# Performance work log

Hardware: AMD Instinct MI355X
Metric: run time of the kernel (lower is better)

The kernel has to match this reference:

```python
import jax, jax.numpy as jnp
import numpy as np

D_MODEL = 1024

def setup_inputs() -> dict:
    key = jax.random.key(0)
    ks = jax.random.split(key, 7)
    scale = 1.0 / np.sqrt(D_MODEL)
    x = jax.random.normal(ks[0], (4, 2048, D_MODEL), dtype=jnp.float32)
    # nn.Linear weights are [out, in]; init uniform(-1/sqrt(in), 1/sqrt(in))
    wq = jax.random.uniform(ks[1], (D_MODEL, D_MODEL), jnp.float32, -scale, scale)
    wk = jax.random.uniform(ks[2], (D_MODEL, D_MODEL), jnp.float32, -scale, scale)
    wv = jax.random.uniform(ks[3], (D_MODEL, D_MODEL), jnp.float32, -scale, scale)
    bq = jax.random.uniform(ks[4], (D_MODEL,), jnp.float32, -scale, scale)
    bk = jax.random.uniform(ks[5], (D_MODEL,), jnp.float32, -scale, scale)
    bv = jax.random.uniform(ks[6], (D_MODEL,), jnp.float32, -scale, scale)
    return {"x": x, "wq": wq, "bq": bq, "wk": wk, "bk": bk, "wv": wv, "bv": bv}

def reference(x, wq, bq, wk, bk, wv, bv):
    B, T, C = x.shape
    q = jnp.einsum('btc,dc->btd', x, wq) + bq  # Linear: x @ W^T + b
    k = jnp.einsum('btc,dc->btd', x, wk) + bk
    v = jnp.einsum('btc,dc->btd', x, wv) + bv
    scores = jnp.einsum('bqd,bkd->bqk', q, k) / jnp.sqrt(jnp.float32(C))
    causal = jnp.tril(jnp.ones((T, T), dtype=bool))  # True = keep
    scores = jnp.where(causal, scores, jnp.finfo(scores.dtype).min)
    attn = jax.nn.softmax(scores, axis=-1)
    return jnp.einsum('bqk,bkd->bqd', attn, v)
```

## Files before the change

### kernel.cpp

```cpp
#include <hip/hip_runtime.h>
#include <math.h>

#define BATCH 4
#define SEQ   2048
#define DM    1024
#define NTOK  (BATCH * SEQ)

typedef __attribute__((ext_vector_type(8))) short bf16x8;
typedef __attribute__((ext_vector_type(4))) float f32x4;
typedef unsigned short u16;
struct alignas(8) us4 { u16 x, y, z, w; };

__device__ __forceinline__ u16 f2bf(float f) {
    union { float f; unsigned u; } v; v.f = f;
    unsigned r = v.u + 0x7fffu + ((v.u >> 16) & 1u);
    return (u16)(r >> 16);
}

__device__ __forceinline__ void gload_lds16(const void* g, void* l) {
    __builtin_amdgcn_global_load_lds(
        (const __attribute__((address_space(1))) unsigned int*)g,
        (__attribute__((address_space(3))) unsigned int*)l, 16, 0, 0);
}

__device__ __forceinline__ void stage_tile(
    const u16* __restrict__ G, int ld, int row0, int kt,
    u16* lds, int wid, int lane)
{
    #pragma unroll
    for (int j = 0; j < 2; ++j) {
        const int off  = wid * 2048 + j * 1024;
        const int loff = off + lane * 16;
        const int row  = loff >> 6;
        const int ke   = (loff & 63) >> 1;
        gload_lds16(G + (size_t)(row0 + row) * ld + kt + ke, (char*)lds + off);
    }
}

__device__ __forceinline__ void frag_mma(
    const u16* As, const u16* Bs, int wr, int wc, int lane, f32x4 acc[4][4])
{
    const int lrow = lane & 15, lk = (lane >> 4) * 8;
    bf16x8 a[4], b[4];
    #pragma unroll
    for (int i = 0; i < 4; ++i)
        a[i] = *(const bf16x8*)(As + (wr * 64 + i * 16 + lrow) * 32 + lk);
    #pragma unroll
    for (int i = 0; i < 4; ++i)
        b[i] = *(const bf16x8*)(Bs + (wc * 64 + i * 16 + lrow) * 32 + lk);
    #pragma unroll
    for (int i = 0; i < 4; ++i)
        #pragma unroll
        for (int j = 0; j < 4; ++j)
            acc[i][j] = __builtin_amdgcn_mfma_f32_16x16x32_bf16(
                a[i], b[j], acc[i][j], 0, 0, 0);
}

__global__ __launch_bounds__(256) void conv_all(
    const float* __restrict__ x,
    const float* __restrict__ w0, const float* __restrict__ w1,
    const float* __restrict__ w2,
    u16* __restrict__ xo,
    u16* __restrict__ o0, u16* __restrict__ o1, u16* __restrict__ o2)
{
    const int z = blockIdx.z;
    const float* in = (z == 0) ? x : (z == 1) ? w0 : (z == 2) ? w1 : w2;
    u16* out = (z == 0) ? xo : (z == 1) ? o0 : (z == 2) ? o1 : o2;
    const int n4 = (z == 0) ? (NTOK * DM / 4) : (DM * DM / 4);
    for (int i = blockIdx.x * 256 + threadIdx.x; i < n4; i += gridDim.x * 256) {
        float4 f = ((const float4*)in)[i];
        us4 p{f2bf(f.x), f2bf(f.y), f2bf(f.z), f2bf(f.w)};
        ((us4*)out)[i] = p;
    }
}

__global__ __launch_bounds__(256, 3) void qkv_mfma(
    const u16* __restrict__ xb,
    const u16* __restrict__ wqb, const float* __restrict__ bq,
    const u16* __restrict__ wkb, const float* __restrict__ bk,
    const u16* __restrict__ wvb, const float* __restrict__ bv,
    u16* __restrict__ qb, u16* __restrict__ kb, u16* __restrict__ vT)
{
    __shared__ u16 As[128 * 32], Bs[128 * 32];
    const int z = blockIdx.z;
    const u16* W = (z == 0) ? wqb : (z == 1) ? wkb : wvb;
    const float* bias = (z == 0) ? bq : (z == 1) ? bk : bv;
    const int m0 = blockIdx.x * 128, n0 = blockIdx.y * 128;
    const int t = threadIdx.x, wid = t >> 6, lane = t & 63;
    const int wr = wid >> 1, wc = wid & 1;

    f32x4 acc[4][4] = {};
    for (int kt = 0; kt < DM; kt += 32) {
        __syncthreads();
        stage_tile(xb, DM, m0, kt, As, wid, lane);
        stage_tile(W,  DM, n0, kt, Bs, wid, lane);
        __syncthreads();
        frag_mma(As, Bs, wr, wc, lane, acc);
    }

    const int lrow = lane & 15, lg = lane >> 4;
    if (z < 2) {
        u16* out = (z == 0) ? qb : kb;
        #pragma unroll
        for (int ni = 0; ni < 4; ++ni) {
            const int n = n0 + wc * 64 + ni * 16 + lrow;
            const float bn = bias[n];
            #pragma unroll
            for (int mi = 0; mi < 4; ++mi) {
                const int mb = m0 + wr * 64 + mi * 16 + lg * 4;
                #pragma unroll
                for (int r = 0; r < 4; ++r)
                    out[(size_t)(mb + r) * DM + n] = f2bf(acc[mi][ni][r] + bn);
            }
        }
    } else {
        #pragma unroll
        for (int ni = 0; ni < 4; ++ni) {
            const int n = n0 + wc * 64 + ni * 16 + lrow;
            const float bn = bias[n];
            #pragma unroll
            for (int mi = 0; mi < 4; ++mi) {
                const int mb = m0 + wr * 64 + mi * 16 + lg * 4;
                us4 p{f2bf(acc[mi][ni][0] + bn), f2bf(acc[mi][ni][1] + bn),
                      f2bf(acc[mi][ni][2] + bn), f2bf(acc[mi][ni][3] + bn)};
                *(us4*)(vT + (size_t)n * NTOK + mb) = p;
            }
        }
    }
}

__global__ __launch_bounds__(256, 3) void qk_exp(
    const u16* __restrict__ qb, const u16* __restrict__ kb,
    u16* __restrict__ attn, float* __restrict__ psum)
{
    const int m0 = blockIdx.x * 128, n0 = blockIdx.y * 128;
    if (n0 > m0) return;
    __shared__ u16 As[128 * 32], Bs[128 * 32];
    const int b = blockIdx.z;
    const u16* A = qb + (size_t)b * SEQ * DM;
    const u16* B = kb + (size_t)b * SEQ * DM;
    u16* P = attn + (size_t)b * SEQ * SEQ;
    const int t = threadIdx.x, wid = t >> 6, lane = t & 63;
    const int wr = wid >> 1, wc = wid & 1;

    f32x4 acc[4][4] = {};
    for (int kt = 0; kt < DM; kt += 32) {
        __syncthreads();
        stage_tile(A, DM, m0, kt, As, wid, lane);
        stage_tile(B, DM, n0, kt, Bs, wid, lane);
        __syncthreads();
        frag_mma(As, Bs, wr, wc, lane, acc);
    }
    const int lrow = lane & 15, lg = lane >> 4;
    const float scale = 0.03125f;
    const int nb = (n0 >> 6) | wc;
    #pragma unroll
    for (int mi = 0; mi < 4; ++mi) {
        #pragma unroll
        for (int r = 0; r < 4; ++r) {
            const int row = m0 + wr * 64 + mi * 16 + lg * 4 + r;
            float ps = 0.f;
            #pragma unroll
            for (int ni = 0; ni < 4; ++ni) {
                const int n = n0 + wc * 64 + ni * 16 + lrow;
                const float p = (n <= row) ? __expf(acc[mi][ni][r] * scale) : 0.f;
                P[(size_t)row * SEQ + n] = f2bf(p);
                ps += p;
            }
            #pragma unroll
            for (int mk = 1; mk < 16; mk <<= 1) ps += __shfl_xor(ps, mk);
            if (lrow == 0)
                psum[((size_t)b * SEQ + row) * 32 + nb] = ps;
        }
    }
}

__global__ __launch_bounds__(256, 3) void pv_mfma(
    const u16* __restrict__ attn, const u16* __restrict__ vT,
    const float* __restrict__ psum, float* __restrict__ out)
{
    __shared__ u16 As[128 * 32], Bs[128 * 32];
    __shared__ float invs[128];
    const int m0 = blockIdx.x * 128, n0 = blockIdx.y * 128;
    const int b = blockIdx.z;
    const u16* A = attn + (size_t)b * SEQ * SEQ;
    const u16* B = vT + (size_t)b * SEQ;
    float* C = out + (size_t)b * SEQ * DM;
    const int t = threadIdx.x, wid = t >> 6, lane = t & 63;
    const int wr = wid >> 1, wc = wid & 1;

    if (t < 128) {
        const int row = m0 + t;
        const float* pr = psum + ((size_t)b * SEQ + row) * 32;
        const int nbmax = (row >> 6) | 1;
        float s = 0.f;
        for (int nbi = 0; nbi <= nbmax; ++nbi) s += pr[nbi];
        invs[t] = 1.f / s;
    }

    f32x4 acc[4][4] = {};
    const int kmax = m0 + 128;
    for (int kt = 0; kt < kmax; kt += 32) {
        __syncthreads();
        stage_tile(A, SEQ,  m0, kt, As, wid, lane);
        stage_tile(B, NTOK, n0, kt, Bs, wid, lane);
        __syncthreads();
        frag_mma(As, Bs, wr, wc, lane, acc);
    }
    const int lrow = lane & 15, lg = lane >> 4;
    #pragma unroll
    for (int mi = 0; mi < 4; ++mi) {
        const int ml = wr * 64 + mi * 16 + lg * 4;
        #pragma unroll
        for (int ni = 0; ni < 4; ++ni) {
            const int n = n0 + wc * 64 + ni * 16 + lrow;
            #pragma unroll
            for (int r = 0; r < 4; ++r)
                C[(size_t)(m0 + ml + r) * DM + n] = acc[mi][ni][r] * invs[ml + r];
        }
    }
}

extern "C" void kernel_launch(void* const* d_in, const int* in_sizes, int n_in,
                              void* d_out, int out_size, void* d_ws, size_t ws_size,
                              hipStream_t stream)
{
    const float* x  = (const float*)d_in[0];
    const float* wq = (const float*)d_in[1];
    const float* bq = (const float*)d_in[2];
    const float* wk = (const float*)d_in[3];
    const float* bk = (const float*)d_in[4];
    const float* wv = (const float*)d_in[5];
    const float* bv = (const float*)d_in[6];
    float* out = (float*)d_out;

    u16* ws  = (u16*)d_ws;
    u16* xb  = ws;
    u16* wqb = xb  + (size_t)NTOK * DM;
    u16* wkb = wqb + (size_t)DM * DM;
    u16* wvb = wkb + (size_t)DM * DM;
    u16* qb  = wvb + (size_t)DM * DM;
    u16* kb  = qb  + (size_t)NTOK * DM;
    u16* vT  = kb  + (size_t)NTOK * DM;
    u16* attn = vT + (size_t)NTOK * DM;
    float* psum = (float*)(attn + (size_t)BATCH * SEQ * SEQ);

    conv_all<<<dim3(512, 1, 4), 256, 0, stream>>>(
        x, wq, wk, wv, xb, wqb, wkb, wvb);

    qkv_mfma<<<dim3(NTOK / 128, DM / 128, 3), 256, 0, stream>>>(
        xb, wqb, bq, wkb, bk, wvb, bv, qb, kb, vT);

    qk_exp<<<dim3(SEQ / 128, SEQ / 128, BATCH), 256, 0, stream>>>(
        qb, kb, attn, psum);

    pv_mfma<<<dim3(SEQ / 128, DM / 128, BATCH), 256, 0, stream>>>(
        attn, vT, psum, out);
}
```

Before: 177.9 us.

## Rewrite QKV projection GEMM as 256x128 double-buffered 8-wave pipelined kernel

Replaces the 128x128, single-buffered QKV projection kernel with a 512-thread kernel computing 256x128 tiles using a K-step of 64. It double-buffers shared memory, uses XOR-swizzled LDS layouts and overlaps async global-to-LDS loads with MFMA phases through explicit vmcnt waits, barriers and setprio. The aim is to hide load latency, cut LDS bank conflicts and raise reuse per tile in the largest GEMM. The cost is more LDS per block, lower occupancy, and hand-tuned waitcnt logic that must stay correct.

Result: slower. 188.9 us (+6.2%).

```diff
diff --git a/kernel.cpp b/kernel.cpp
--- a/kernel.cpp
+++ b/kernel.cpp
@@ -22,6 +22,163 @@
         (const __attribute__((address_space(1))) unsigned int*)g,
         (__attribute__((address_space(3))) unsigned int*)l, 16, 0, 0);
 }
+
+
+__device__ __forceinline__ void stageA(const u16* __restrict__ G, int ld,
+    int row0, int kt, u16* Ab, int h, int wid, int lane)
+{
+    #pragma unroll
+    for (int rr = 0; rr < 2; ++rr) {
+        const int base = h * 16384 + rr * 8192 + wid * 1024;
+        const int off  = base + lane * 16;
+        const int row  = off >> 7;
+        const int cbs  = (off & 127) ^ ((row & 7) << 4);
+        gload_lds16(G + (size_t)(row0 + row) * ld + kt + (cbs >> 1),
+                    (char*)Ab + base);
+    }
+}
+__device__ __forceinline__ void stageB(const u16* __restrict__ G, int ld,
+    int row0, int kt, u16* Bb, int h, int wid, int lane)
+{
+    const int base = h * 8192 + wid * 1024;
+    const int off  = base + lane * 16;
+    const int row  = off >> 7;
+    const int cbs  = (off & 127) ^ ((row & 7) << 4);
+    gload_lds16(G + (size_t)(row0 + row) * ld + kt + (cbs >> 1),
+                (char*)Bb + base);
+}
+
+struct Frags { bf16x8 a[2][4]; bf16x8 b[2]; };
+
+template<int MH, int NH>
+__device__ __forceinline__ Frags phase_read(const u16* As, const u16* Bs,
+                                            int wr, int wc, int lane)
+{
+    Frags fr;
+    const int lrow = lane & 15, lhi = lane >> 4, sw = (lane & 7) << 4;
+    #pragma unroll
+    for (int kk = 0; kk < 2; ++kk) {
+        const int cb = (kk * 64 + lhi * 16) ^ sw;
+        #pragma unroll
+        for (int fi = 0; fi < 4; ++fi) {
+            const int row = (2 * (MH * 4 + fi) + wr) * 16 + lrow;
+            fr.a[kk][fi] = *(const bf16x8*)(As + row * 64 + (cb >> 1));
+        }
+        const int nrow = (4 * NH + wc) * 16 + lrow;
+        fr.b[kk] = *(const bf16x8*)(Bs + nrow * 64 + (cb >> 1));
+    }
+    return fr;
+}
+
+template<int MH, int NH>
+__device__ __forceinline__ void phase_fma(const Frags& fr, f32x4 acc[8][2])
+{
+    __builtin_amdgcn_s_setprio(1);
+    #pragma unroll
+    for (int fi = 0; fi < 4; ++fi)
+        #pragma unroll
+        for (int kk = 0; kk < 2; ++kk)
+            acc[MH * 4 + fi][NH] = __builtin_amdgcn_mfma_f32_16x16x32_bf16(
+                fr.a[kk][fi], fr.b[kk], acc[MH * 4 + fi][NH], 0, 0, 0);
+    __builtin_amdgcn_s_setprio(0);
+}
+
+#define VM3 asm volatile("s_waitcnt vmcnt(3)" ::: "memory")
+#define VM0 asm volatile("s_waitcnt vmcnt(0)" ::: "memory")
+#define BAR __builtin_amdgcn_s_barrier()
+
+__global__ __launch_bounds__(512) void qkv_mfma8(
+    const u16* __restrict__ xb,
+    const u16* __restrict__ wqb, const float* __restrict__ bq,
+    const u16* __restrict__ wkb, const float* __restrict__ bk,
+    const u16* __restrict__ wvb, const float* __restrict__ bv,
+    u16* __restrict__ qb, u16* __restrict__ kb, u16* __restrict__ vT)
+{
+    __shared__ u16 As0[256 * 64], As1[256 * 64];
+    __shared__ u16 Bs0[128 * 64], Bs1[128 * 64];
+
+    const int z = blockIdx.z;
+    const u16* W = (z == 0) ? wqb : (z == 1) ? wkb : wvb;
+    const float* bias = (z == 0) ? bq : (z == 1) ? bk : bv;
+    const int m0 = blockIdx.x * 256;
+    const int n0 = blockIdx.y * 128;
+    const int t = threadIdx.x, wid = t >> 6, lane = t & 63;
+    const int wr = wid >> 2, wc = wid & 3;
+
+    f32x4 acc[8][2] = {};
+
+    stageA(xb, DM, m0, 0,  As0, 0, wid, lane);
+    stageB(W,  DM, n0, 0,  Bs0, 0, wid, lane);
+    stageA(xb, DM, m0, 0,  As0, 1, wid, lane);
+    stageB(W,  DM, n0, 0,  Bs0, 1, wid, lane);
+    stageA(xb, DM, m0, 64, As1, 0, wid, lane);
+    stageB(W,  DM, n0, 64, Bs1, 0, wid, lane);
+    VM3;
+    BAR;
+
+    #pragma unroll 1
+    for (int i = 0; i < 8; ++i) {
+        const int kb2 = i * 128 + 64, k2 = i * 128 + 128, k3 = i * 128 + 192;
+        const bool s2 = (k2 < 1024), s3 = (k3 < 1024);
+        { Frags fr = phase_read<0,0>(As0, Bs0, wr, wc, lane);
+          stageA(xb, DM, m0, kb2, As1, 1, wid, lane);
+          BAR; phase_fma<0,0>(fr, acc); BAR; }
+        { Frags fr = phase_read<0,1>(As0, Bs0, wr, wc, lane);
+          stageB(W, DM, n0, kb2, Bs1, 1, wid, lane);
+          BAR; phase_fma<0,1>(fr, acc); BAR; }
+        { Frags fr = phase_read<1,0>(As0, Bs0, wr, wc, lane);
+          if (s2) stageA(xb, DM, m0, k2, As0, 0, wid, lane);
+          BAR; phase_fma<1,0>(fr, acc); BAR; }
+        { Frags fr = phase_read<1,1>(As0, Bs0, wr, wc, lane);
+          if (s2) { stageB(W, DM, n0, k2, Bs0, 0, wid, lane); VM3; }
+          else    { VM0; }
+          BAR; phase_fma<1,1>(fr, acc); BAR; }
+        { Frags fr = phase_read<0,0>(As1, Bs1, wr, wc, lane);
+          if (s2) stageA(xb, DM, m0, k2, As0, 1, wid, lane);
+          BAR; phase_fma<0,0>(fr, acc); BAR; }
+        { Frags fr = phase_read<0,1>(As1, Bs1, wr, wc, lane);
+          if (s2) stageB(W, DM, n0, k2, Bs0, 1, wid, lane);
+          BAR; phase_fma<0,1>(fr, acc); BAR; }
+        { Frags fr = phase_read<1,0>(As1, Bs1, wr, wc, lane);
+          if (s3) stageA(xb, DM, m0, k3, As1, 0, wid, lane);
+          BAR; phase_fma<1,0>(fr, acc); BAR; }
+        { Frags fr = phase_read<1,1>(As1, Bs1, wr, wc, lane);
+          if (s3) { stageB(W, DM, n0, k3, Bs1, 0, wid, lane); VM3; }
+          else    { VM0; }
+          BAR; phase_fma<1,1>(fr, acc); BAR; }
+    }
+
+    const int lrow = lane & 15, lhi = lane >> 4;
+    if (z < 2) {
+        u16* outp = (z == 0) ? qb : kb;
+        #pragma unroll
+        for (int g = 0; g < 2; ++g) {
+            const int n = n0 + (4 * g + wc) * 16 + lrow;
+            const float bn = bias[n];
+            #pragma unroll
+            for (int f = 0; f < 8; ++f) {
+                const int mb = m0 + (2 * f + wr) * 16 + lhi * 4;
+                #pragma unroll
+                for (int r = 0; r < 4; ++r)
+                    outp[(size_t)(mb + r) * DM + n] = f2bf(acc[f][g][r] + bn);
+            }
+        }
+    } else {
+        #pragma unroll
+        for (int g = 0; g < 2; ++g) {
+            const int n = n0 + (4 * g + wc) * 16 + lrow;
+            const float bn = bias[n];
+            #pragma unroll
+            for (int f = 0; f < 8; ++f) {
+                const int mb = m0 + (2 * f + wr) * 16 + lhi * 4;
+                us4 p{f2bf(acc[f][g][0] + bn), f2bf(acc[f][g][1] + bn),
+                      f2bf(acc[f][g][2] + bn), f2bf(acc[f][g][3] + bn)};
+                *(us4*)(vT + (size_t)n * NTOK + mb) = p;
+            }
+        }
+    }
+}
+
 
 __device__ __forceinline__ void stage_tile(
     const u16* __restrict__ G, int ld, int row0, int kt,
@@ -71,61 +228,6 @@
         float4 f = ((const float4*)in)[i];
         us4 p{f2bf(f.x), f2bf(f.y), f2bf(f.z), f2bf(f.w)};
         ((us4*)out)[i] = p;
-    }
-}
-
-__global__ __launch_bounds__(256, 3) void qkv_mfma(
-    const u16* __restrict__ xb,
-    const u16* __restrict__ wqb, const float* __restrict__ bq,
-    const u16* __restrict__ wkb, const float* __restrict__ bk,
-    const u16* __restrict__ wvb, const float* __restrict__ bv,
-    u16* __restrict__ qb, u16* __restrict__ kb, u16* __restrict__ vT)
-{
-    __shared__ u16 As[128 * 32], Bs[128 * 32];
-    const int z = blockIdx.z;
-    const u16* W = (z == 0) ? wqb : (z == 1) ? wkb : wvb;
-    const float* bias = (z == 0) ? bq : (z == 1) ? bk : bv;
-    const int m0 = blockIdx.x * 128, n0 = blockIdx.y * 128;
-    const int t = threadIdx.x, wid = t >> 6, lane = t & 63;
-    const int wr = wid >> 1, wc = wid & 1;
-
-    f32x4 acc[4][4] = {};
-    for (int kt = 0; kt < DM; kt += 32) {
-        __syncthreads();
-        stage_tile(xb, DM, m0, kt, As, wid, lane);
-        stage_tile(W,  DM, n0, kt, Bs, wid, lane);
-        __syncthreads();
-        frag_mma(As, Bs, wr, wc, lane, acc);
-    }
-
-    const int lrow = lane & 15, lg = lane >> 4;
-    if (z < 2) {
-        u16* out = (z == 0) ? qb : kb;
-        #pragma unroll
-        for (int ni = 0; ni < 4; ++ni) {
-            const int n = n0 + wc * 64 + ni * 16 + lrow;
-            const float bn = bias[n];
-            #pragma unroll
-            for (int mi = 0; mi < 4; ++mi) {
-                const int mb = m0 + wr * 64 + mi * 16 + lg * 4;
-                #pragma unroll
-                for (int r = 0; r < 4; ++r)
-                    out[(size_t)(mb + r) * DM + n] = f2bf(acc[mi][ni][r] + bn);
-            }
-        }
-    } else {
-        #pragma unroll
-        for (int ni = 0; ni < 4; ++ni) {
-            const int n = n0 + wc * 64 + ni * 16 + lrow;
-            const float bn = bias[n];
-            #pragma unroll
-            for (int mi = 0; mi < 4; ++mi) {
-                const int mb = m0 + wr * 64 + mi * 16 + lg * 4;
-                us4 p{f2bf(acc[mi][ni][0] + bn), f2bf(acc[mi][ni][1] + bn),
-                      f2bf(acc[mi][ni][2] + bn), f2bf(acc[mi][ni][3] + bn)};
-                *(us4*)(vT + (size_t)n * NTOK + mb) = p;
-            }
-        }
     }
 }
 
@@ -248,7 +350,7 @@
     conv_all<<<dim3(512, 1, 4), 256, 0, stream>>>(
         x, wq, wk, wv, xb, wqb, wkb, wvb);
 
-    qkv_mfma<<<dim3(NTOK / 128, DM / 128, 3), 256, 0, stream>>>(
+    qkv_mfma8<<<dim3(NTOK / 256, 8, 3), 512, 0, stream>>>(
         xb, wqb, bq, wkb, bk, wvb, bv, qb, kb, vT);
 
     qk_exp<<<dim3(SEQ / 128, SEQ / 128, BATCH), 256, 0, stream>>>(
```

## Enlarge GEMM tiles to 128x256 with BK=64 and XOR-swizzled LDS

Applied to the files above, without the earlier changes.

All three MFMA GEMM kernels (QKV projection, QK^T with exp, PV) move from 128x128 tiles with a K-step of 32 to 128x256 tiles with a K-step of 64. Each wave now computes a 64x128 sub-tile, which doubles MFMA work per LDS fragment load and halves the number of barrier pairs. LDS rows are XOR-swizzled in both the async global-to-LDS staging and the fragment reads to avoid bank conflicts. The cost is more accumulator registers, 48KB of LDS per block, dropped occupancy hints, and coarser causal tiles in qk_exp, which compute more masked-out work.

After: 233.9 us. 1.32x slower.

```diff
diff --git a/kernel.cpp b/kernel.cpp
--- a/kernel.cpp
+++ b/kernel.cpp
@@ -23,37 +23,48 @@
         (__attribute__((address_space(3))) unsigned int*)l, 16, 0, 0);
 }
 
-__device__ __forceinline__ void stage_tile(
-    const u16* __restrict__ G, int ld, int row0, int kt,
-    u16* lds, int wid, int lane)
-{
-    #pragma unroll
-    for (int j = 0; j < 2; ++j) {
-        const int off  = wid * 2048 + j * 1024;
-        const int loff = off + lane * 16;
-        const int row  = loff >> 6;
-        const int ke   = (loff & 63) >> 1;
-        gload_lds16(G + (size_t)(row0 + row) * ld + kt + ke, (char*)lds + off);
-    }
-}
-
-__device__ __forceinline__ void frag_mma(
-    const u16* As, const u16* Bs, int wr, int wc, int lane, f32x4 acc[4][4])
-{
-    const int lrow = lane & 15, lk = (lane >> 4) * 8;
-    bf16x8 a[4], b[4];
-    #pragma unroll
-    for (int i = 0; i < 4; ++i)
-        a[i] = *(const bf16x8*)(As + (wr * 64 + i * 16 + lrow) * 32 + lk);
-    #pragma unroll
-    for (int i = 0; i < 4; ++i)
-        b[i] = *(const bf16x8*)(Bs + (wc * 64 + i * 16 + lrow) * 32 + lk);
-    #pragma unroll
-    for (int i = 0; i < 4; ++i)
-        #pragma unroll
-        for (int j = 0; j < 4; ++j)
-            acc[i][j] = __builtin_amdgcn_mfma_f32_16x16x32_bf16(
-                a[i], b[j], acc[i][j], 0, 0, 0);
+
+__device__ __forceinline__ void stage64(const u16* __restrict__ G, int ld,
+    int row0, int kt, u16* lds, int wid, int lane)
+{
+    #pragma unroll
+    for (int j = 0; j < 4; ++j) {
+        const int base = j * 4096 + wid * 1024;
+        const int off  = base + lane * 16;
+        const int row  = off >> 7;
+        const int colb = (off & 127) ^ ((row & 7) << 4);
+        gload_lds16(G + (size_t)(row0 + row) * ld + kt + (colb >> 1),
+                    (char*)lds + base);
+    }
+}
+
+__device__ __forceinline__ bf16x8 ldsF(const u16* T, int frow, int kk, int lane)
+{
+    const int row  = frow * 16 + (lane & 15);
+    const int colb = (kk * 64 + ((lane >> 4) << 4)) ^ ((row & 7) << 4);
+    return *(const bf16x8*)(T + row * 64 + (colb >> 1));
+}
+
+__device__ __forceinline__ void tile_fma(const u16* As, const u16* Bs,
+                                         int wid, int lane, f32x4 acc[4][8])
+{
+    const int fa = (wid >> 1) * 4;
+    const int fb = (wid & 1) * 8;
+    #pragma unroll
+    for (int kk = 0; kk < 2; ++kk) {
+        bf16x8 a0 = ldsF(As, fa + 0, kk, lane);
+        bf16x8 a1 = ldsF(As, fa + 1, kk, lane);
+        bf16x8 a2 = ldsF(As, fa + 2, kk, lane);
+        bf16x8 a3 = ldsF(As, fa + 3, kk, lane);
+        #pragma unroll
+        for (int nf = 0; nf < 8; ++nf) {
+            bf16x8 b = ldsF(Bs, fb + nf, kk, lane);
+            acc[0][nf] = __builtin_amdgcn_mfma_f32_16x16x32_bf16(a0, b, acc[0][nf], 0, 0, 0);
+            acc[1][nf] = __builtin_amdgcn_mfma_f32_16x16x32_bf16(a1, b, acc[1][nf], 0, 0, 0);
+            acc[2][nf] = __builtin_amdgcn_mfma_f32_16x16x32_bf16(a2, b, acc[2][nf], 0, 0, 0);
+            acc[3][nf] = __builtin_amdgcn_mfma_f32_16x16x32_bf16(a3, b, acc[3][nf], 0, 0, 0);
+        }
+    }
 }
 
 __global__ __launch_bounds__(256) void conv_all(
@@ -74,120 +85,127 @@
     }
 }
 
-__global__ __launch_bounds__(256, 3) void qkv_mfma(
+__global__ __launch_bounds__(256) void qkv_mfma(
     const u16* __restrict__ xb,
     const u16* __restrict__ wqb, const float* __restrict__ bq,
     const u16* __restrict__ wkb, const float* __restrict__ bk,
     const u16* __restrict__ wvb, const float* __restrict__ bv,
     u16* __restrict__ qb, u16* __restrict__ kb, u16* __restrict__ vT)
 {
-    __shared__ u16 As[128 * 32], Bs[128 * 32];
+    __shared__ u16 As[128 * 64], Bs[256 * 64];
     const int z = blockIdx.z;
     const u16* W = (z == 0) ? wqb : (z == 1) ? wkb : wvb;
     const float* bias = (z == 0) ? bq : (z == 1) ? bk : bv;
-    const int m0 = blockIdx.x * 128, n0 = blockIdx.y * 128;
+    const int m0 = blockIdx.x * 128, n0 = blockIdx.y * 256;
     const int t = threadIdx.x, wid = t >> 6, lane = t & 63;
-    const int wr = wid >> 1, wc = wid & 1;
-
-    f32x4 acc[4][4] = {};
-    for (int kt = 0; kt < DM; kt += 32) {
-        __syncthreads();
-        stage_tile(xb, DM, m0, kt, As, wid, lane);
-        stage_tile(W,  DM, n0, kt, Bs, wid, lane);
-        __syncthreads();
-        frag_mma(As, Bs, wr, wc, lane, acc);
-    }
-
-    const int lrow = lane & 15, lg = lane >> 4;
+
+    f32x4 acc[4][8] = {};
+    for (int kt = 0; kt < DM; kt += 64) {
+        __syncthreads();
+        stage64(xb, DM, m0, kt, As, wid, lane);
+        stage64(W,  DM, n0,       kt, Bs,            wid, lane);
+        stage64(W,  DM, n0 + 128, kt, Bs + 128 * 64, wid, lane);
+        __syncthreads();
+        tile_fma(As, Bs, wid, lane, acc);
+    }
+
+    const int lrow = lane & 15, lhi = lane >> 4;
+    const int Mb = m0 + (wid >> 1) * 64, Nb = n0 + (wid & 1) * 128;
     if (z < 2) {
-        u16* out = (z == 0) ? qb : kb;
-        #pragma unroll
-        for (int ni = 0; ni < 4; ++ni) {
-            const int n = n0 + wc * 64 + ni * 16 + lrow;
+        u16* outp = (z == 0) ? qb : kb;
+        #pragma unroll
+        for (int nf = 0; nf < 8; ++nf) {
+            const int n = Nb + nf * 16 + lrow;
             const float bn = bias[n];
             #pragma unroll
             for (int mi = 0; mi < 4; ++mi) {
-                const int mb = m0 + wr * 64 + mi * 16 + lg * 4;
+                const int mb = Mb + mi * 16 + lhi * 4;
                 #pragma unroll
                 for (int r = 0; r < 4; ++r)
-                    out[(size_t)(mb + r) * DM + n] = f2bf(acc[mi][ni][r] + bn);
+                    outp[(size_t)(mb + r) * DM + n] = f2bf(acc[mi][nf][r] + bn);
             }
         }
     } else {
         #pragma unroll
-        for (int ni = 0; ni < 4; ++ni) {
-            const int n = n0 + wc * 64 + ni * 16 + lrow;
+        for (int nf = 0; nf < 8; ++nf) {
+            const int n = Nb + nf * 16 + lrow;
             const float bn = bias[n];
             #pragma unroll
             for (int mi = 0; mi < 4; ++mi) {
-                const int mb = m0 + wr * 64 + mi * 16 + lg * 4;
-                us4 p{f2bf(acc[mi][ni][0] + bn), f2bf(acc[mi][ni][1] + bn),
-                      f2bf(acc[mi][ni][2] + bn), f2bf(acc[mi][ni][3] + bn)};
+                const int mb = Mb + mi * 16 + lhi * 4;
+                us4 p{f2bf(acc[mi][nf][0] + bn), f2bf(acc[mi][nf][1] + bn),
+                      f2bf(acc[mi][nf][2] + bn), f2bf(acc[mi][nf][3] + bn)};
                 *(us4*)(vT + (size_t)n * NTOK + mb) = p;
             }
         }
     }
 }
 
-__global__ __launch_bounds__(256, 3) void qk_exp(
+__global__ __launch_bounds__(256) void qk_exp(
     const u16* __restrict__ qb, const u16* __restrict__ kb,
     u16* __restrict__ attn, float* __restrict__ psum)
 {
-    const int m0 = blockIdx.x * 128, n0 = blockIdx.y * 128;
+    const int m0 = blockIdx.x * 128, n0 = blockIdx.y * 256;
     if (n0 > m0) return;
-    __shared__ u16 As[128 * 32], Bs[128 * 32];
+    __shared__ u16 As[128 * 64], Bs[256 * 64];
     const int b = blockIdx.z;
     const u16* A = qb + (size_t)b * SEQ * DM;
     const u16* B = kb + (size_t)b * SEQ * DM;
     u16* P = attn + (size_t)b * SEQ * SEQ;
     const int t = threadIdx.x, wid = t >> 6, lane = t & 63;
-    const int wr = wid >> 1, wc = wid & 1;
-
-    f32x4 acc[4][4] = {};
-    for (int kt = 0; kt < DM; kt += 32) {
-        __syncthreads();
-        stage_tile(A, DM, m0, kt, As, wid, lane);
-        stage_tile(B, DM, n0, kt, Bs, wid, lane);
-        __syncthreads();
-        frag_mma(As, Bs, wr, wc, lane, acc);
-    }
-    const int lrow = lane & 15, lg = lane >> 4;
+
+    f32x4 acc[4][8] = {};
+    for (int kt = 0; kt < DM; kt += 64) {
+        __syncthreads();
+        stage64(A, DM, m0, kt, As, wid, lane);
+        stage64(B, DM, n0,       kt, Bs,            wid, lane);
+        stage64(B, DM, n0 + 128, kt, Bs + 128 * 64, wid, lane);
+        __syncthreads();
+        tile_fma(As, Bs, wid, lane, acc);
+    }
+
+    const int lrow = lane & 15, lhi = lane >> 4;
+    const int Mb = m0 + (wid >> 1) * 64, Nb = n0 + (wid & 1) * 128;
     const float scale = 0.03125f;
-    const int nb = (n0 >> 6) | wc;
+    const int nb0 = Nb >> 6;
     #pragma unroll
     for (int mi = 0; mi < 4; ++mi) {
         #pragma unroll
         for (int r = 0; r < 4; ++r) {
-            const int row = m0 + wr * 64 + mi * 16 + lg * 4 + r;
-            float ps = 0.f;
-            #pragma unroll
-            for (int ni = 0; ni < 4; ++ni) {
-                const int n = n0 + wc * 64 + ni * 16 + lrow;
-                const float p = (n <= row) ? __expf(acc[mi][ni][r] * scale) : 0.f;
+            const int row = Mb + mi * 16 + lhi * 4 + r;
+            float ps0 = 0.f, ps1 = 0.f;
+            #pragma unroll
+            for (int nf = 0; nf < 8; ++nf) {
+                const int n = Nb + nf * 16 + lrow;
+                const float p = (n <= row) ? __expf(acc[mi][nf][r] * scale) : 0.f;
                 P[(size_t)row * SEQ + n] = f2bf(p);
-                ps += p;
-            }
-            #pragma unroll
-            for (int mk = 1; mk < 16; mk <<= 1) ps += __shfl_xor(ps, mk);
-            if (lrow == 0)
-                psum[((size_t)b * SEQ + row) * 32 + nb] = ps;
-        }
-    }
-}
-
-__global__ __launch_bounds__(256, 3) void pv_mfma(
+                if (nf < 4) ps0 += p; else ps1 += p;
+            }
+            #pragma unroll
+            for (int mk = 1; mk < 16; mk <<= 1) {
+                ps0 += __shfl_xor(ps0, mk);
+                ps1 += __shfl_xor(ps1, mk);
+            }
+            if (lrow == 0) {
+                psum[((size_t)b * SEQ + row) * 32 + nb0]     = ps0;
+                psum[((size_t)b * SEQ + row) * 32 + nb0 + 1] = ps1;
+            }
+        }
+    }
+}
+
+__global__ __launch_bounds__(256) void pv_mfma(
     const u16* __restrict__ attn, const u16* __restrict__ vT,
     const float* __restrict__ psum, float* __restrict__ out)
 {
-    __shared__ u16 As[128 * 32], Bs[128 * 32];
+    __shared__ u16 As[128 * 64], Bs[256 * 64];
     __shared__ float invs[128];
-    const int m0 = blockIdx.x * 128, n0 = blockIdx.y * 128;
+    const int m0 = blockIdx.x * 128, n0 = blockIdx.y * 256;
     const int b = blockIdx.z;
     const u16* A = attn + (size_t)b * SEQ * SEQ;
     const u16* B = vT + (size_t)b * SEQ;
     float* C = out + (size_t)b * SEQ * DM;
     const int t = threadIdx.x, wid = t >> 6, lane = t & 63;
-    const int wr = wid >> 1, wc = wid & 1;
 
     if (t < 128) {
         const int row = m0 + t;
@@ -198,25 +216,28 @@
         invs[t] = 1.f / s;
     }
 
-    f32x4 acc[4][4] = {};
+    f32x4 acc[4][8] = {};
     const int kmax = m0 + 128;
-    for (int kt = 0; kt < kmax; kt += 32) {
-        __syncthreads();
-        stage_tile(A, SEQ,  m0, kt, As, wid, lane);
-        stage_tile(B, NTOK, n0, kt, Bs, wid, lane);
-        __syncthreads();
-        frag_mma(As, Bs, wr, wc, lane, acc);
-    }
-    const int lrow = lane & 15, lg = lane >> 4;
+    for (int kt = 0; kt < kmax; kt += 64) {
+        __syncthreads();
+        stage64(A, SEQ,  m0, kt, As, wid, lane);
+        stage64(B, NTOK, n0,       kt, Bs,            wid, lane);
+        stage64(B, NTOK, n0 + 128, kt, Bs + 128 * 64, wid, lane);
+        __syncthreads();
+        tile_fma(As, Bs, wid, lane, acc);
+    }
+
+    const int lrow = lane & 15, lhi = lane >> 4;
+    const int Mb = (wid >> 1) * 64, Nb = n0 + (wid & 1) * 128;
     #pragma unroll
     for (int mi = 0; mi < 4; ++mi) {
-        const int ml = wr * 64 + mi * 16 + lg * 4;
-        #pragma unroll
-        for (int ni = 0; ni < 4; ++ni) {
-            const int n = n0 + wc * 64 + ni * 16 + lrow;
+        const int ml = Mb + mi * 16 + lhi * 4;
+        #pragma unroll
+        for (int nf = 0; nf < 8; ++nf) {
+            const int n = Nb + nf * 16 + lrow;
             #pragma unroll
             for (int r = 0; r < 4; ++r)
-                C[(size_t)(m0 + ml + r) * DM + n] = acc[mi][ni][r] * invs[ml + r];
+                C[(size_t)(m0 + ml + r) * DM + n] = acc[mi][nf][r] * invs[ml + r];
         }
     }
 }
@@ -248,12 +269,12 @@
     conv_all<<<dim3(512, 1, 4), 256, 0, stream>>>(
         x, wq, wk, wv, xb, wqb, wkb, wvb);
 
-    qkv_mfma<<<dim3(NTOK / 128, DM / 128, 3), 256, 0, stream>>>(
+    qkv_mfma<<<dim3(NTOK / 128, DM / 256, 3), 256, 0, stream>>>(
         xb, wqb, bq, wkb, bk, wvb, bv, qb, kb, vT);
 
-    qk_exp<<<dim3(SEQ / 128, SEQ / 128, BATCH), 256, 0, stream>>>(
+    qk_exp<<<dim3(SEQ / 128, SEQ / 256, BATCH), 256, 0, stream>>>(
         qb, kb, attn, psum);
 
-    pv_mfma<<<dim3(SEQ / 128, DM / 128, BATCH), 256, 0, stream>>>(
+    pv_mfma<<<dim3(SEQ / 128, DM / 256, BATCH), 256, 0, stream>>>(
         attn, vT, psum, out);
 }
```

## Replace QKV projection GEMM with 256x256 pipelined 8-wave MFMA kernel

Applied to the files above, without the earlier changes.

Swaps the simple 128x128 QKV projection kernel for a 256x256-tile, 512-thread kernel. It double-buffers 128 KB of LDS with an XOR swizzle, issues global-to-LDS loads in quarter steps interleaved with MFMA phases, and uses vmcnt waits and raw barriers in place of full __syncthreads. The aim is to hide global load latency, raise data reuse per tile and avoid LDS bank conflicts. The costs are lower occupancy, a large LDS footprint and fragile hand-placed synchronisation.

New measurement: 173.4 us. 2.5% less time.

```diff
diff --git a/kernel.cpp b/kernel.cpp
--- a/kernel.cpp
+++ b/kernel.cpp
@@ -22,6 +22,157 @@
         (const __attribute__((address_space(1))) unsigned int*)g,
         (__attribute__((address_space(3))) unsigned int*)l, 16, 0, 0);
 }
+
+#define VM6 asm volatile("s_waitcnt vmcnt(6)" ::: "memory")
+#define BAR __builtin_amdgcn_s_barrier()
+
+
+__device__ __forceinline__ void stageH(const u16* __restrict__ G, int ld,
+    int row0, int kt, u16* half_lds, int wid, int lane)
+{
+    #pragma unroll
+    for (int j = 0; j < 2; ++j) {
+        const int base = j * 8192 + wid * 1024;
+        const int off  = base + lane * 16;
+        const int row  = off >> 7;
+        const int colb = (off & 127) ^ ((row & 7) << 4);
+        gload_lds16(G + (size_t)(row0 + row) * ld + kt + (colb >> 1),
+                    (char*)half_lds + base);
+    }
+}
+
+__device__ __forceinline__ bf16x8 ldsF(const u16* T, int fr, int kk, int lane)
+{
+    const int row  = fr * 16 + (lane & 15);
+    const int colb = (kk * 64 + ((lane >> 4) << 4)) ^ ((row & 7) << 4);
+    return *(const bf16x8*)(T + row * 64 + (colb >> 1));
+}
+
+template<int MB, int NB>
+__device__ __forceinline__ void mma16(const bf16x8 A[4][2], const bf16x8 B[2][2],
+                                      f32x4 acc[8][4])
+{
+    __builtin_amdgcn_s_setprio(1);
+    #pragma unroll
+    for (int i = 0; i < 4; ++i)
+        #pragma unroll
+        for (int j = 0; j < 2; ++j)
+            #pragma unroll
+            for (int kk = 0; kk < 2; ++kk)
+                acc[MB + i][NB + j] = __builtin_amdgcn_mfma_f32_16x16x32_bf16(
+                    A[i][kk], B[j][kk], acc[MB + i][NB + j], 0, 0, 0);
+    __builtin_amdgcn_s_setprio(0);
+}
+
+__global__ __launch_bounds__(512, 2) void qkv_mfma8(
+    const u16* __restrict__ xb,
+    const u16* __restrict__ wqb, const float* __restrict__ bq,
+    const u16* __restrict__ wkb, const float* __restrict__ bk,
+    const u16* __restrict__ wvb, const float* __restrict__ bv,
+    u16* __restrict__ qb, u16* __restrict__ kb, u16* __restrict__ vT)
+{
+    __shared__ alignas(16) u16 LDS[65536];
+    const int z = blockIdx.z;
+    const u16* W = (z == 0) ? wqb : (z == 1) ? wkb : wvb;
+    const float* bias = (z == 0) ? bq : (z == 1) ? bk : bv;
+    const int m0 = blockIdx.x * 256, n0 = blockIdx.y * 256;
+    const int t = threadIdx.x, wid = t >> 6, lane = t & 63;
+    const int wm = wid >> 2, wn = wid & 3;
+
+    f32x4 acc[8][4] = {};
+
+    stageH(xb, DM, m0,       0,  LDS + 0,             wid, lane);
+    stageH(W,  DM, n0,       0,  LDS + 32768,         wid, lane);
+    stageH(xb, DM, m0 + 128, 0,  LDS + 8192,          wid, lane);
+    stageH(W,  DM, n0 + 128, 0,  LDS + 32768 + 8192,  wid, lane);
+    stageH(xb, DM, m0,       64, LDS + 16384,         wid, lane);
+    VM6;
+    BAR;
+
+    bf16x8 rA0[4][2], rA1[4][2], rB[2][2];
+
+    #pragma unroll 1
+    for (int ti = 0; ti < 16; ++ti) {
+        const int cur = ti & 1, nxt = cur ^ 1;
+        u16* Ac0 = LDS + cur * 16384;
+        u16* Ac1 = Ac0 + 8192;
+        u16* Bc0 = LDS + 32768 + cur * 16384;
+        u16* Bc1 = Bc0 + 8192;
+        u16* An0_t2 = LDS + cur * 16384;
+        u16* An1    = LDS + nxt * 16384 + 8192;
+        u16* Bn0    = LDS + 32768 + nxt * 16384;
+        u16* Bn1    = Bn0 + 8192;
+        const int kt1 = (ti + 1) < 16 ? (ti + 1) * 64 : 0;
+        const int kt2 = (ti + 2) < 16 ? (ti + 2) * 64 : 0;
+
+        #pragma unroll
+        for (int i = 0; i < 4; ++i) {
+            rA0[i][0] = ldsF(Ac0, 2 * i + wm, 0, lane);
+            rA0[i][1] = ldsF(Ac0, 2 * i + wm, 1, lane);
+        }
+        #pragma unroll
+        for (int j = 0; j < 2; ++j) {
+            rB[j][0] = ldsF(Bc0, 4 * j + wn, 0, lane);
+            rB[j][1] = ldsF(Bc0, 4 * j + wn, 1, lane);
+        }
+        stageH(W, DM, n0, kt1, Bn0, wid, lane);
+        VM6; BAR;
+        mma16<0, 0>(rA0, rB, acc);
+
+        #pragma unroll
+        for (int i = 0; i < 4; ++i) {
+            rA1[i][0] = ldsF(Ac1, 2 * i + wm, 0, lane);
+            rA1[i][1] = ldsF(Ac1, 2 * i + wm, 1, lane);
+        }
+        stageH(xb, DM, m0 + 128, kt1, An1, wid, lane);
+        VM6; BAR;
+        mma16<4, 0>(rA1, rB, acc);
+
+        #pragma unroll
+        for (int j = 0; j < 2; ++j) {
+            rB[j][0] = ldsF(Bc1, 4 * j + wn, 0, lane);
+            rB[j][1] = ldsF(Bc1, 4 * j + wn, 1, lane);
+        }
+        stageH(W, DM, n0 + 128, kt1, Bn1, wid, lane);
+        VM6; BAR;
+        mma16<4, 2>(rA1, rB, acc);
+
+        stageH(xb, DM, m0, kt2, An0_t2, wid, lane);
+        VM6; BAR;
+        mma16<0, 2>(rA0, rB, acc);
+    }
+
+    const int lrow = lane & 15, lhi = lane >> 4;
+    if (z < 2) {
+        u16* outp = (z == 0) ? qb : kb;
+        #pragma unroll
+        for (int nf = 0; nf < 4; ++nf) {
+            const int n = n0 + (4 * nf + wn) * 16 + lrow;
+            const float bn = bias[n];
+            #pragma unroll
+            for (int mf = 0; mf < 8; ++mf) {
+                const int mb = m0 + (2 * mf + wm) * 16 + lhi * 4;
+                #pragma unroll
+                for (int r = 0; r < 4; ++r)
+                    outp[(size_t)(mb + r) * DM + n] = f2bf(acc[mf][nf][r] + bn);
+            }
+        }
+    } else {
+        #pragma unroll
+        for (int nf = 0; nf < 4; ++nf) {
+            const int n = n0 + (4 * nf + wn) * 16 + lrow;
+            const float bn = bias[n];
+            #pragma unroll
+            for (int mf = 0; mf < 8; ++mf) {
+                const int mb = m0 + (2 * mf + wm) * 16 + lhi * 4;
+                us4 p{f2bf(acc[mf][nf][0] + bn), f2bf(acc[mf][nf][1] + bn),
+                      f2bf(acc[mf][nf][2] + bn), f2bf(acc[mf][nf][3] + bn)};
+                *(us4*)(vT + (size_t)n * NTOK + mb) = p;
+            }
+        }
+    }
+}
+
 
 __device__ __forceinline__ void stage_tile(
     const u16* __restrict__ G, int ld, int row0, int kt,
@@ -71,61 +222,6 @@
         float4 f = ((const float4*)in)[i];
         us4 p{f2bf(f.x), f2bf(f.y), f2bf(f.z), f2bf(f.w)};
         ((us4*)out)[i] = p;
-    }
-}
-
-__global__ __launch_bounds__(256, 3) void qkv_mfma(
-    const u16* __restrict__ xb,
-    const u16* __restrict__ wqb, const float* __restrict__ bq,
-    const u16* __restrict__ wkb, const float* __restrict__ bk,
-    const u16* __restrict__ wvb, const float* __restrict__ bv,
-    u16* __restrict__ qb, u16* __restrict__ kb, u16* __restrict__ vT)
-{
-    __shared__ u16 As[128 * 32], Bs[128 * 32];
-    const int z = blockIdx.z;
-    const u16* W = (z == 0) ? wqb : (z == 1) ? wkb : wvb;
-    const float* bias = (z == 0) ? bq : (z == 1) ? bk : bv;
-    const int m0 = blockIdx.x * 128, n0 = blockIdx.y * 128;
-    const int t = threadIdx.x, wid = t >> 6, lane = t & 63;
-    const int wr = wid >> 1, wc = wid & 1;
-
-    f32x4 acc[4][4] = {};
-    for (int kt = 0; kt < DM; kt += 32) {
-        __syncthreads();
-        stage_tile(xb, DM, m0, kt, As, wid, lane);
-        stage_tile(W,  DM, n0, kt, Bs, wid, lane);
-        __syncthreads();
-        frag_mma(As, Bs, wr, wc, lane, acc);
-    }
-
-    const int lrow = lane & 15, lg = lane >> 4;
-    if (z < 2) {
-        u16* out = (z == 0) ? qb : kb;
-        #pragma unroll
-        for (int ni = 0; ni < 4; ++ni) {
-            const int n = n0 + wc * 64 + ni * 16 + lrow;
-            const float bn = bias[n];
-            #pragma unroll
-            for (int mi = 0; mi < 4; ++mi) {
-                const int mb = m0 + wr * 64 + mi * 16 + lg * 4;
-                #pragma unroll
-                for (int r = 0; r < 4; ++r)
-                    out[(size_t)(mb + r) * DM + n] = f2bf(acc[mi][ni][r] + bn);
-            }
-        }
-    } else {
-        #pragma unroll
-        for (int ni = 0; ni < 4; ++ni) {
-            const int n = n0 + wc * 64 + ni * 16 + lrow;
-            const float bn = bias[n];
-            #pragma unroll
-            for (int mi = 0; mi < 4; ++mi) {
-                const int mb = m0 + wr * 64 + mi * 16 + lg * 4;
-                us4 p{f2bf(acc[mi][ni][0] + bn), f2bf(acc[mi][ni][1] + bn),
-                      f2bf(acc[mi][ni][2] + bn), f2bf(acc[mi][ni][3] + bn)};
-                *(us4*)(vT + (size_t)n * NTOK + mb) = p;
-            }
-        }
     }
 }
 
@@ -248,7 +344,7 @@
     conv_all<<<dim3(512, 1, 4), 256, 0, stream>>>(
         x, wq, wk, wv, xb, wqb, wkb, wvb);
 
-    qkv_mfma<<<dim3(NTOK / 128, DM / 128, 3), 256, 0, stream>>>(
+    qkv_mfma8<<<dim3(NTOK / 256, DM / 256, 3), 512, 0, stream>>>(
         xb, wqb, bq, wkb, bk, wvb, bv, qb, kb, vT);
 
     qk_exp<<<dim3(SEQ / 128, SEQ / 128, BATCH), 256, 0, stream>>>(
```
